# Kernel tuning notes

Hardware: AMD Instinct MI355X
Metric: run time of the kernel (lower is better)

## Reference

```python
import math
import jax, jax.numpy as jnp
import numpy as np


def get_slopes(n):
    def pow2(n):
        start = 2.0 ** (-(2.0 ** (-(math.log2(n) - 3))))
        return [start * (start ** i) for i in range(n)]
    if math.log2(n).is_integer():
        return pow2(n)
    c = 2 ** math.floor(math.log2(n))
    return pow2(c) + get_slopes(2 * c)[0::2][: n - c]


def setup_inputs() -> dict:
    key = jax.random.key(0)
    B, T, C = 2, 2048, 1024
    ks = jax.random.split(key, 9)
    std = 0.02
    n_layers = 12
    inp = {
        "x": jax.random.normal(ks[0], (B, T, C), dtype=jnp.float32),
        # weights stored as [in, out] (transpose of torch Linear.weight)
        "Wq": std * jax.random.normal(ks[1], (C, C), dtype=jnp.float32),
        "bq": jnp.zeros((C,), dtype=jnp.float32),
        "Wk": std * jax.random.normal(ks[2], (C, C), dtype=jnp.float32),
        "bk": jnp.zeros((C,), dtype=jnp.float32),
        "Wv": std * jax.random.normal(ks[3], (C, C), dtype=jnp.float32),
        "bv": jnp.zeros((C,), dtype=jnp.float32),
        # fc_resid gets std 0.02/sqrt(2*num_layers)
        "Wo": (std / math.sqrt(2 * n_layers)) * jax.random.normal(ks[4], (C, C), dtype=jnp.float32),
        "bo": jnp.zeros((C,), dtype=jnp.float32),
        "n_head": 16,
    }
    return inp


def reference(x, Wq, bq, Wk, bk, Wv, bv, Wo, bo, n_head):
    B, T, C = x.shape
    hd = C // n_head
    # QKV projections, split heads: [B, nh, T, hd]
    def proj(W, b):
        return (x @ W + b).reshape(B, T, n_head, hd).transpose(0, 2, 1, 3)
    q, k, v = proj(Wq, bq), proj(Wk, bk), proj(Wv, bv)

    # ALiBi bias: bias[h, i, j] = -slope_h * (i - j) for j <= i, -inf above diag
    slopes = jnp.asarray(get_slopes(n_head), dtype=x.dtype)  # [nh]
    idx = jnp.arange(T)
    dist = (idx[:, None] - idx[None, :]).astype(x.dtype)  # [T, T], i - j
    bias = -slopes[:, None, None] * dist  # [nh, T, T]
    causal = idx[:, None] >= idx[None, :]
    bias = jnp.where(causal[None], bias, jnp.asarray(-jnp.inf, dtype=x.dtype))

    scale = 1.0 / math.sqrt(hd)
    scores = jnp.einsum("bnqh,bnkh->bnqk", q, k) * scale + bias[None]
    att = jax.nn.softmax(scores, axis=-1)
    y = jnp.einsum("bnqk,bnkh->bnqh", att, v)  # [B, nh, T, hd]
    y = y.transpose(0, 2, 1, 3).reshape(B, T, C)
    return y @ Wo + bo
```

## Files before the change

kernel.cpp:

```cpp
#include <hip/hip_runtime.h>


typedef unsigned short u16;
typedef unsigned int u32;
typedef __attribute__((ext_vector_type(8))) short bf16x8;
typedef __attribute__((ext_vector_type(4))) float f32x4;
typedef __attribute__((ext_vector_type(4))) unsigned short u16x4;

#define MFMA16x16(A, B, C_) __builtin_amdgcn_mfma_f32_16x16x32_bf16((A), (B), (C_), 0, 0, 0)

__device__ __forceinline__ u16 f2bf(float f) {
  u32 x = __builtin_bit_cast(u32, f);
  x += 0x7fff + ((x >> 16) & 1);
  return (u16)(x >> 16);
}

__device__ __forceinline__ void gload_lds16(const u16* g, u16* l) {
  __builtin_amdgcn_global_load_lds(
      (const __attribute__((address_space(1))) void*)g,
      (__attribute__((address_space(3))) void*)l, 16, 0, 0);
}

constexpr int T = 2048, C = 1024, HD = 64;
constexpr int BT = 2 * T;

__device__ __forceinline__ bf16x8 ldsfrag(const u16* lds, int row, int kchunk) {
  return *(const bf16x8*)(lds + row * 64 + (((kchunk) ^ (row & 7)) << 3));
}

__global__ __launch_bounds__(256) void convert_x_kernel(
    const float* __restrict__ xin, u16* __restrict__ xc) {
  int i = (blockIdx.x * 256 + threadIdx.x) * 8;
  const float4 a = *(const float4*)(xin + i);
  const float4 b = *(const float4*)(xin + i + 4);
  uint4 o;
  o.x = (u32)f2bf(a.x) | ((u32)f2bf(a.y) << 16);
  o.y = (u32)f2bf(a.z) | ((u32)f2bf(a.w) << 16);
  o.z = (u32)f2bf(b.x) | ((u32)f2bf(b.y) << 16);
  o.w = (u32)f2bf(b.z) | ((u32)f2bf(b.w) << 16);
  *(uint4*)(xc + i) = o;
}

__global__ __launch_bounds__(256) void transpose4_kernel(
    const float* __restrict__ w0, const float* __restrict__ w1,
    const float* __restrict__ w2, const float* __restrict__ w3,
    u16* __restrict__ wqkvT, u16* __restrict__ woT) {
  __shared__ u16 tile[32][33];
  const int z = blockIdx.z;
  const float* in = (z == 0) ? w0 : (z == 1) ? w1 : (z == 2) ? w2 : w3;
  u16* out = (z < 3) ? (wqkvT + (size_t)z * (1u << 20)) : woT;
  int tx = threadIdx.x, ty = threadIdx.y;
  int x = blockIdx.x * 32 + tx;
#pragma unroll
  for (int i = 0; i < 4; i++) {
    int y = blockIdx.y * 32 + ty + i * 8;
    tile[ty + i * 8][tx] = f2bf(in[y * 1024 + x]);
  }
  __syncthreads();
  int xo = blockIdx.y * 32 + tx;
#pragma unroll
  for (int i = 0; i < 4; i++) {
    int yo = blockIdx.x * 32 + ty + i * 8;
    out[yo * 1024 + xo] = tile[tx][ty + i * 8];
  }
}

__global__ __launch_bounds__(512, 2) void gemm_qkv_kernel(
    const u16* __restrict__ A, const u16* __restrict__ Bt,
    const float* __restrict__ b0, const float* __restrict__ b1,
    const float* __restrict__ b2,
    u16* __restrict__ qout, u16* __restrict__ kout, u16* __restrict__ vtout) {
  constexpr int K = 1024, BK = 32, NT = K / BK;
  __shared__ __align__(16) u16 ring[4][2][256 * BK];

  const int tid = threadIdx.x;
  const int w = tid >> 6, lane = tid & 63;
  const int l15 = lane & 15, quad = lane >> 4;
  const int wr = w >> 2, wc = w & 3;
  const int bid = blockIdx.y * 12 + blockIdx.x;
  const int swz = (bid & 7) * 24 + (bid >> 3);
  const int m0 = (swz / 12) * 256, n0 = (swz % 12) * 256;
  const int rw = lane >> 2;
  const int pc = lane & 3;

  const u16* Ag = A + (size_t)m0 * K;
  const u16* Bg = Bt + (size_t)n0 * K;

  f32x4 acc[8][4] = {};

  auto STAGE = [&](int kt, int s) {
#pragma unroll
    for (int j = 0; j < 2; j++) {
      int row = j * 128 + w * 16 + rw;
      int cl = pc ^ (row & 3);
      gload_lds16(Ag + (size_t)row * K + kt * BK + cl * 8,
                  &ring[s][0][(j * 128 + w * 16) * BK]);
      gload_lds16(Bg + (size_t)row * K + kt * BK + cl * 8,
                  &ring[s][1][(j * 128 + w * 16) * BK]);
    }
  };

  STAGE(0, 0); STAGE(1, 1); STAGE(2, 2);
  asm volatile("s_waitcnt vmcnt(8)" ::: "memory");
  __builtin_amdgcn_s_barrier();

#pragma unroll 1
  for (int t = 0; t < NT; ++t) {
    const int s = t & 3;
    if (t + 3 < NT) STAGE(t + 3, (t + 3) & 3);

    const u16* As = ring[s][0];
    const u16* Bs = ring[s][1];
    bf16x8 bfr[4], afr[8];
#pragma unroll
    for (int ni = 0; ni < 4; ni++) {
      int row = wc * 64 + ni * 16 + l15;
      bfr[ni] = *(const bf16x8*)(Bs + row * BK + ((quad ^ (row & 3)) << 3));
    }
#pragma unroll
    for (int mi = 0; mi < 8; mi++) {
      int row = wr * 128 + mi * 16 + l15;
      afr[mi] = *(const bf16x8*)(As + row * BK + ((quad ^ (row & 3)) << 3));
    }
    __builtin_amdgcn_s_setprio(1);
#pragma unroll
    for (int mi = 0; mi < 8; mi++)
#pragma unroll
      for (int ni = 0; ni < 4; ni++)
        acc[mi][ni] = MFMA16x16(afr[mi], bfr[ni], acc[mi][ni]);
    __builtin_amdgcn_s_setprio(0);

    if (t + 3 < NT)
      asm volatile("s_waitcnt vmcnt(8)" ::: "memory");
    else if (t + 2 < NT)
      asm volatile("s_waitcnt vmcnt(4)" ::: "memory");
    else if (t + 1 < NT)
      asm volatile("s_waitcnt vmcnt(0)" ::: "memory");
    if (t + 1 < NT) __builtin_amdgcn_s_barrier();
  }

  const int sel = n0 >> 10;
  const int nloc = n0 & 1023;
  if (sel < 2) {
    u16* D = (sel == 0) ? qout : kout;
    const float* bias = (sel == 0) ? b0 : b1;
#pragma unroll
    for (int mi = 0; mi < 8; mi++)
#pragma unroll
      for (int ni = 0; ni < 4; ni++) {
        int rb = m0 + wr * 128 + mi * 16 + quad * 4;
        int col = nloc + wc * 64 + ni * 16 + l15;
        float bb = bias[col];
#pragma unroll
        for (int r = 0; r < 4; r++)
          D[(size_t)(rb + r) * 1024 + col] = f2bf(acc[mi][ni][r] + bb);
      }
  } else {
#pragma unroll
    for (int mi = 0; mi < 8; mi++)
#pragma unroll
      for (int ni = 0; ni < 4; ni++) {
        int rb = m0 + wr * 128 + mi * 16 + quad * 4;
        int c = nloc + wc * 64 + ni * 16 + l15;
        float bb = b2[c];
        u16x4 pk;
#pragma unroll
        for (int r = 0; r < 4; r++) pk[r] = f2bf(acc[mi][ni][r] + bb);
        *(u16x4*)(vtout + (size_t)c * 4096 + rb) = pk;
      }
  }
}

__global__ __launch_bounds__(256) void gemm_out_kernel(
    const u16* __restrict__ A, const u16* __restrict__ Bt,
    const float* __restrict__ bias, float* __restrict__ fout) {
  constexpr int K = 1024;
  __shared__ __align__(16) u16 As[128 * 64];
  __shared__ __align__(16) u16 Bs[64 * 64];

  const int tid = threadIdx.x;
  const int w = tid >> 6, lane = tid & 63;
  const int l15 = lane & 15, quad = lane >> 4;
  const int m0 = blockIdx.y * 128, n0 = blockIdx.x * 64;
  const int wm = (w >> 1) * 64, wn = (w & 1) * 32;
  const int gsub = (lane & 7) ^ ((lane >> 3) & 7);
  const int rsub = lane >> 3;

  f32x4 acc[4][2] = {};
  const u16* Ag = A + (size_t)m0 * K;
  const u16* Bg = Bt + (size_t)n0 * K;

  for (int k0 = 0; k0 < K; k0 += 64) {
    __syncthreads();
#pragma unroll
    for (int t = 0; t < 4; t++) {
      int rbase = w * 32 + t * 8;
      gload_lds16(Ag + (size_t)(rbase + rsub) * K + k0 + gsub * 8, As + rbase * 64);
    }
#pragma unroll
    for (int t = 0; t < 2; t++) {
      int rbase = w * 16 + t * 8;
      gload_lds16(Bg + (size_t)(rbase + rsub) * K + k0 + gsub * 8, Bs + rbase * 64);
    }
    __syncthreads();
#pragma unroll
    for (int ks = 0; ks < 2; ks++) {
      bf16x8 af[4], bf[2];
#pragma unroll
      for (int mi = 0; mi < 4; mi++)
        af[mi] = ldsfrag(As, wm + mi * 16 + l15, (ks << 2) | quad);
#pragma unroll
      for (int ni = 0; ni < 2; ni++)
        bf[ni] = ldsfrag(Bs, wn + ni * 16 + l15, (ks << 2) | quad);
#pragma unroll
      for (int mi = 0; mi < 4; mi++)
#pragma unroll
        for (int ni = 0; ni < 2; ni++)
          acc[mi][ni] = MFMA16x16(af[mi], bf[ni], acc[mi][ni]);
    }
  }

#pragma unroll
  for (int mi = 0; mi < 4; mi++)
#pragma unroll
    for (int ni = 0; ni < 2; ni++) {
      int rb = m0 + wm + mi * 16 + quad * 4;
      int col = n0 + wn + ni * 16 + l15;
      float bb = bias[col];
#pragma unroll
      for (int r = 0; r < 4; r++)
        fout[(size_t)(rb + r) * 1024 + col] = acc[mi][ni][r] + bb;
    }
}

__global__ __launch_bounds__(512, 4) void attn_kernel(
    const u16* __restrict__ qbuf, const u16* __restrict__ kbuf,
    const u16* __restrict__ vtbuf, u16* __restrict__ ybuf) {
  __shared__ __align__(16) u16 Qs[64 * 64];
  __shared__ __align__(16) u16 KVs[4][64 * 64];
  __shared__ __align__(16) u16 Ps[8][16 * 64];

  const int tid = threadIdx.x;
  const int w = tid >> 6, lane = tid & 63;
  const int wq = w & 3, g = w >> 2;
  const int l15 = lane & 15, quad = lane >> 4;
  const int bh = blockIdx.y, b = bh >> 4, h = bh & 15;
  const float slope = exp2f(-0.5f * (float)(h + 1));
  const float slope128 = slope * 128.f;
  const int gsub = (lane & 7) ^ ((lane >> 3) & 7);
  const int rsub = lane >> 3;

  const u16* kbase0 = kbuf + (size_t)b * T * C + h * HD;
  const u16* vtbase0 = vtbuf + (size_t)h * HD * BT + (size_t)b * T;
  u16* Pw = Ps[w];
  const int st = w >> 1;
  const int skind = st & 1;
  const int sjt = st >> 1;
  const int srb = (w & 1) * 32;

#pragma unroll 1
  for (int half = 0; half < 2; half++) {
    const int qt = half == 0 ? (31 - (int)blockIdx.x) : (int)blockIdx.x;

    __syncthreads();
    const u16* qb = qbuf + (size_t)(b * T + qt * 64) * C + h * HD;
    gload_lds16(qb + (size_t)(w * 8 + rsub) * C + gsub * 8, Qs + (w * 8) * 64);
    __syncthreads();
    bf16x8 aq0 = ldsfrag(Qs, wq * 16 + l15, quad);
    bf16x8 aq1 = ldsfrag(Qs, wq * 16 + l15, 4 + quad);

    f32x4 o[4] = {};
    float lsum[4] = {0.f, 0.f, 0.f, 0.f};
    float br[4][4];
    const int ig0 = qt * 64 + wq * 16 + quad * 4;
#pragma unroll
    for (int ni = 0; ni < 4; ni++)
#pragma unroll
      for (int r = 0; r < 4; r++)
        br[ni][r] = slope * (float)(g * 64 + ni * 16 + l15 - ig0 - r);

    const int iters = (qt + 2) >> 1;
#pragma unroll 1
    for (int it = 0; it < iters; it++) {
      __syncthreads();
      {
        int jtv = 2 * it + sjt;
        int jtr = jtv > qt ? qt : jtv;
        const u16* base = skind ? (vtbase0 + jtr * 64)
                                : (kbase0 + (size_t)jtr * 64 * C);
        const int stride = skind ? BT : C;
        u16* dst = KVs[skind * 2 + sjt] + srb * 64;
#pragma unroll
        for (int c2 = 0; c2 < 4; c2++)
          gload_lds16(base + (size_t)(srb + c2 * 8 + rsub) * stride + gsub * 8,
                      dst + c2 * 8 * 64);
      }
      __syncthreads();

      const int jtv = 2 * it + g;
      const u16* Kw = KVs[g];
      const u16* Vw = KVs[2 + g];

      f32x4 s[4];
#pragma unroll
      for (int ni = 0; ni < 4; ni++) {
        bf16x8 kf0 = ldsfrag(Kw, ni * 16 + l15, quad);
        bf16x8 kf1 = ldsfrag(Kw, ni * 16 + l15, 4 + quad);
        f32x4 z = {0.f, 0.f, 0.f, 0.f};
        z = MFMA16x16(aq0, kf0, z);
        z = MFMA16x16(aq1, kf1, z);
        s[ni] = z;
      }

      const bool edge = (jtv >= qt);
#pragma unroll
      for (int ni = 0; ni < 4; ni++)
#pragma unroll
        for (int r = 0; r < 4; r++) {
          float p = __expf(fmaf(s[ni][r], 0.125f, br[ni][r]));
          if (edge && (jtv * 64 + ni * 16 + l15) > (ig0 + r)) p = 0.f;
          lsum[r] += p;
          int prow = quad * 4 + r, pcol = ni * 16 + l15;
          Pw[prow * 64 + (((pcol >> 3) ^ (prow & 7)) << 3) + (pcol & 7)] = f2bf(p);
          br[ni][r] += slope128;
        }

      bf16x8 pa0 = ldsfrag(Pw, l15, quad);
      bf16x8 pa1 = ldsfrag(Pw, l15, 4 + quad);
#pragma unroll
      for (int ni = 0; ni < 4; ni++) {
        bf16x8 vf0 = ldsfrag(Vw, ni * 16 + l15, quad);
        bf16x8 vf1 = ldsfrag(Vw, ni * 16 + l15, 4 + quad);
        o[ni] = MFMA16x16(pa0, vf0, o[ni]);
        o[ni] = MFMA16x16(pa1, vf1, o[ni]);
      }
    }

    __syncthreads();
    float* sc = (float*)KVs;
    float* Osc = sc + wq * 1024;
    float* Lsc = sc + 4096 + wq * 256;
    if (g == 1) {
#pragma unroll
      for (int ni = 0; ni < 4; ni++)
#pragma unroll
        for (int r = 0; r < 4; r++)
          Osc[(quad * 4 + r) * 64 + ni * 16 + l15] = o[ni][r];
#pragma unroll
      for (int r = 0; r < 4; r++)
        Lsc[(quad * 4 + r) * 16 + l15] = lsum[r];
    }
    __syncthreads();
    if (g == 0) {
#pragma unroll
      for (int ni = 0; ni < 4; ni++)
#pragma unroll
        for (int r = 0; r < 4; r++)
          o[ni][r] += Osc[(quad * 4 + r) * 64 + ni * 16 + l15];
#pragma unroll
      for (int r = 0; r < 4; r++) {
        float l = lsum[r] + Lsc[(quad * 4 + r) * 16 + l15];
        l += __shfl_xor(l, 1);
        l += __shfl_xor(l, 2);
        l += __shfl_xor(l, 4);
        l += __shfl_xor(l, 8);
        float inv = 1.f / l;
        int row_g = b * T + qt * 64 + wq * 16 + quad * 4 + r;
        u16* yrow = ybuf + (size_t)row_g * C + h * HD;
#pragma unroll
        for (int ni = 0; ni < 4; ni++)
          yrow[ni * 16 + l15] = f2bf(o[ni][r] * inv);
      }
    }
  }
}

extern "C" void kernel_launch(void* const* d_in, const int* in_sizes, int n_in,
                              void* d_out, int out_size, void* d_ws, size_t ws_size,
                              hipStream_t stream) {
  (void)in_sizes; (void)n_in; (void)out_size; (void)ws_size;
  const float* x  = (const float*)d_in[0];
  const float* Wq = (const float*)d_in[1];
  const float* bq = (const float*)d_in[2];
  const float* Wk = (const float*)d_in[3];
  const float* bk = (const float*)d_in[4];
  const float* Wv = (const float*)d_in[5];
  const float* bv = (const float*)d_in[6];
  const float* Wo = (const float*)d_in[7];
  const float* bo = (const float*)d_in[8];

  u16* ws = (u16*)d_ws;
  constexpr size_t M1 = 1u << 20;
  u16* wqkvT = ws;
  u16* woT   = ws + 3 * M1;
  u16* xc    = ws + 4 * M1;
  u16* qbuf  = ws + 8 * M1;
  u16* vtbuf = ws + 12 * M1;
  u16* kbuf  = (u16*)d_out;
  u16* ybuf  = qbuf;

  convert_x_kernel<<<2048, 256, 0, stream>>>(x, xc);
  transpose4_kernel<<<dim3(32, 32, 4), dim3(32, 8), 0, stream>>>(Wq, Wk, Wv, Wo, wqkvT, woT);
  gemm_qkv_kernel<<<dim3(12, 16), 512, 0, stream>>>(
      xc, wqkvT, bq, bk, bv, qbuf, kbuf, vtbuf);
  attn_kernel<<<dim3(16, 32), 512, 0, stream>>>(qbuf, kbuf, vtbuf, ybuf);
  gemm_out_kernel<<<dim3(16, 32), 256, 0, stream>>>(ybuf, woT, bo, (float*)d_out);
}
```

Before: 196.5 us.

## Fuse prep kernels and streamline attention loop with exp2, peeled masking, priorities

```diff
diff --git a/kernel.cpp b/kernel.cpp
--- a/kernel.cpp
+++ b/kernel.cpp
@@ -28,39 +28,42 @@
   return *(const bf16x8*)(lds + row * 64 + (((kchunk) ^ (row & 7)) << 3));
 }
 
-__global__ __launch_bounds__(256) void convert_x_kernel(
-    const float* __restrict__ xin, u16* __restrict__ xc) {
-  int i = (blockIdx.x * 256 + threadIdx.x) * 8;
-  const float4 a = *(const float4*)(xin + i);
-  const float4 b = *(const float4*)(xin + i + 4);
-  uint4 o;
-  o.x = (u32)f2bf(a.x) | ((u32)f2bf(a.y) << 16);
-  o.y = (u32)f2bf(a.z) | ((u32)f2bf(a.w) << 16);
-  o.z = (u32)f2bf(b.x) | ((u32)f2bf(b.y) << 16);
-  o.w = (u32)f2bf(b.z) | ((u32)f2bf(b.w) << 16);
-  *(uint4*)(xc + i) = o;
-}
-
-__global__ __launch_bounds__(256) void transpose4_kernel(
+__global__ __launch_bounds__(256) void prep_kernel(
+    const float* __restrict__ xin, u16* __restrict__ xc,
     const float* __restrict__ w0, const float* __restrict__ w1,
     const float* __restrict__ w2, const float* __restrict__ w3,
     u16* __restrict__ wqkvT, u16* __restrict__ woT) {
   __shared__ u16 tile[32][33];
-  const int z = blockIdx.z;
+  const int bz = blockIdx.x, tid = threadIdx.x;
+  if (bz < 2048) {
+    int i = (bz * 256 + tid) * 8;
+    const float4 a = *(const float4*)(xin + i);
+    const float4 b = *(const float4*)(xin + i + 4);
+    uint4 o;
+    o.x = (u32)f2bf(a.x) | ((u32)f2bf(a.y) << 16);
+    o.y = (u32)f2bf(a.z) | ((u32)f2bf(a.w) << 16);
+    o.z = (u32)f2bf(b.x) | ((u32)f2bf(b.y) << 16);
+    o.w = (u32)f2bf(b.z) | ((u32)f2bf(b.w) << 16);
+    *(uint4*)(xc + i) = o;
+    return;
+  }
+  const int t = bz - 2048;
+  const int z = t >> 10, rem = t & 1023;
+  const int bx = rem & 31, by = rem >> 5;
   const float* in = (z == 0) ? w0 : (z == 1) ? w1 : (z == 2) ? w2 : w3;
   u16* out = (z < 3) ? (wqkvT + (size_t)z * (1u << 20)) : woT;
-  int tx = threadIdx.x, ty = threadIdx.y;
-  int x = blockIdx.x * 32 + tx;
+  const int tx = tid & 31, ty = tid >> 5;
+  int x = bx * 32 + tx;
 #pragma unroll
   for (int i = 0; i < 4; i++) {
-    int y = blockIdx.y * 32 + ty + i * 8;
+    int y = by * 32 + ty + i * 8;
     tile[ty + i * 8][tx] = f2bf(in[y * 1024 + x]);
   }
   __syncthreads();
-  int xo = blockIdx.y * 32 + tx;
+  int xo = by * 32 + tx;
 #pragma unroll
   for (int i = 0; i < 4; i++) {
-    int yo = blockIdx.x * 32 + ty + i * 8;
+    int yo = bx * 32 + ty + i * 8;
     out[yo * 1024 + xo] = tile[tx][ty + i * 8];
   }
 }
@@ -233,10 +236,9 @@
     }
 }
 
-__global__ __launch_bounds__(512, 4) void attn_kernel(
+__global__ __launch_bounds__(512, 6) void attn_kernel(
     const u16* __restrict__ qbuf, const u16* __restrict__ kbuf,
     const u16* __restrict__ vtbuf, u16* __restrict__ ybuf) {
-  __shared__ __align__(16) u16 Qs[64 * 64];
   __shared__ __align__(16) u16 KVs[4][64 * 64];
   __shared__ __align__(16) u16 Ps[8][16 * 64];
 
@@ -245,8 +247,9 @@
   const int wq = w & 3, g = w >> 2;
   const int l15 = lane & 15, quad = lane >> 4;
   const int bh = blockIdx.y, b = bh >> 4, h = bh & 15;
-  const float slope = exp2f(-0.5f * (float)(h + 1));
-  const float slope128 = slope * 128.f;
+  constexpr float LOG2E = 1.44269504f;
+  const float slope2 = exp2f(-0.5f * (float)(h + 1)) * LOG2E;
+  const float slope128 = slope2 * 128.f;
   const int gsub = (lane & 7) ^ ((lane >> 3) & 7);
   const int rsub = lane >> 3;
 
@@ -262,12 +265,9 @@
   for (int half = 0; half < 2; half++) {
     const int qt = half == 0 ? (31 - (int)blockIdx.x) : (int)blockIdx.x;
 
-    __syncthreads();
-    const u16* qb = qbuf + (size_t)(b * T + qt * 64) * C + h * HD;
-    gload_lds16(qb + (size_t)(w * 8 + rsub) * C + gsub * 8, Qs + (w * 8) * 64);
-    __syncthreads();
-    bf16x8 aq0 = ldsfrag(Qs, wq * 16 + l15, quad);
-    bf16x8 aq1 = ldsfrag(Qs, wq * 16 + l15, 4 + quad);
+    const u16* qb = qbuf + (size_t)(b * T + qt * 64 + wq * 16 + l15) * C + h * HD;
+    bf16x8 aq0 = *(const bf16x8*)(qb + quad * 8);
+    bf16x8 aq1 = *(const bf16x8*)(qb + 32 + quad * 8);
 
     f32x4 o[4] = {};
     float lsum[4] = {0.f, 0.f, 0.f, 0.f};
@@ -277,11 +277,9 @@
     for (int ni = 0; ni < 4; ni++)
 #pragma unroll
       for (int r = 0; r < 4; r++)
-        br[ni][r] = slope * (float)(g * 64 + ni * 16 + l15 - ig0 - r);
-
-    const int iters = (qt + 2) >> 1;
-#pragma unroll 1
-    for (int it = 0; it < iters; it++) {
+        br[ni][r] = slope2 * (float)(g * 64 + ni * 16 + l15 - ig0 - r);
+
+    auto tile_body = [&](int it, int masked) {
       __syncthreads();
       {
         int jtv = 2 * it + sjt;
@@ -302,6 +300,7 @@
       const u16* Vw = KVs[2 + g];
 
       f32x4 s[4];
+      __builtin_amdgcn_s_setprio(1);
 #pragma unroll
       for (int ni = 0; ni < 4; ni++) {
         bf16x8 kf0 = ldsfrag(Kw, ni * 16 + l15, quad);
@@ -311,14 +310,16 @@
         z = MFMA16x16(aq1, kf1, z);
         s[ni] = z;
       }
-
-      const bool edge = (jtv >= qt);
+      __builtin_amdgcn_s_setprio(0);
+
 #pragma unroll
       for (int ni = 0; ni < 4; ni++)
 #pragma unroll
         for (int r = 0; r < 4; r++) {
-          float p = __expf(fmaf(s[ni][r], 0.125f, br[ni][r]));
-          if (edge && (jtv * 64 + ni * 16 + l15) > (ig0 + r)) p = 0.f;
+          float p = exp2f(fmaf(s[ni][r], 0.125f * LOG2E, br[ni][r]));
+          if (masked) {
+            if ((jtv >= qt) && (jtv * 64 + ni * 16 + l15) > (ig0 + r)) p = 0.f;
+          }
           lsum[r] += p;
           int prow = quad * 4 + r, pcol = ni * 16 + l15;
           Pw[prow * 64 + (((pcol >> 3) ^ (prow & 7)) << 3) + (pcol & 7)] = f2bf(p);
@@ -327,6 +328,7 @@
 
       bf16x8 pa0 = ldsfrag(Pw, l15, quad);
       bf16x8 pa1 = ldsfrag(Pw, l15, 4 + quad);
+      __builtin_amdgcn_s_setprio(1);
 #pragma unroll
       for (int ni = 0; ni < 4; ni++) {
         bf16x8 vf0 = ldsfrag(Vw, ni * 16 + l15, quad);
@@ -334,7 +336,13 @@
         o[ni] = MFMA16x16(pa0, vf0, o[ni]);
         o[ni] = MFMA16x16(pa1, vf1, o[ni]);
       }
-    }
+      __builtin_amdgcn_s_setprio(0);
+    };
+
+    const int iters = (qt + 2) >> 1;
+#pragma unroll 1
+    for (int it = 0; it < iters - 1; it++) tile_body(it, 0);
+    tile_body(iters - 1, 1);
 
     __syncthreads();
     float* sc = (float*)KVs;
@@ -399,8 +407,7 @@
   u16* kbuf  = (u16*)d_out;
   u16* ybuf  = qbuf;
 
-  convert_x_kernel<<<2048, 256, 0, stream>>>(x, xc);
-  transpose4_kernel<<<dim3(32, 32, 4), dim3(32, 8), 0, stream>>>(Wq, Wk, Wv, Wo, wqkvT, woT);
+  prep_kernel<<<6144, 256, 0, stream>>>(x, xc, Wq, Wk, Wv, Wo, wqkvT, woT);
   gemm_qkv_kernel<<<dim3(12, 16), 512, 0, stream>>>(
       xc, wqkvT, bq, bk, bv, qbuf, kbuf, vtbuf);
   attn_kernel<<<dim3(16, 32), 512, 0, stream>>>(qbuf, kbuf, vtbuf, ybuf);
```

Result: slower. 301.5 us (+53.5%).
